# Performance work log

Hardware: AMD Instinct MI355X
Metric: run time of the kernel (lower is better)

The kernel has to match this reference:

```python
import jax, jax.numpy as jnp
import numpy as np

N_TYPES = 4
N_RELS = 8
N, E, IN_DIM, OUT_DIM = 100000, 1600000, 64, 64
SQRT_DK = float(np.sqrt(OUT_DIM))  # num_heads = 1 -> d_k = out_dim


def setup_inputs() -> dict:
    key = jax.random.key(0)
    ks = jax.random.split(key, 12)
    s = 0.05  # keep activations well-scaled (xavier-ish)
    h = jax.random.normal(ks[0], (N, IN_DIM), jnp.float32)
    node_type = jax.random.randint(ks[1], (N,), 0, N_TYPES, jnp.int32)
    src = jax.random.randint(ks[2], (E,), 0, N, jnp.int32)
    dst = jax.random.randint(ks[3], (E,), 0, N, jnp.int32)
    etype = jax.random.randint(ks[4], (E,), 0, N_RELS, jnp.int32)
    k_lin = jax.random.normal(ks[5], (N_TYPES, IN_DIM, OUT_DIM), jnp.float32) * s
    q_lin = jax.random.normal(ks[6], (N_TYPES, IN_DIM, OUT_DIM), jnp.float32) * s
    v_lin = jax.random.normal(ks[7], (N_TYPES, IN_DIM, OUT_DIM), jnp.float32) * s
    a_lin = jax.random.normal(ks[8], (N_TYPES, OUT_DIM, OUT_DIM), jnp.float32) * s
    rel_att = jax.random.normal(ks[9], (N_RELS, OUT_DIM, OUT_DIM), jnp.float32) * s
    rel_msg = jax.random.normal(ks[10], (N_RELS, OUT_DIM, OUT_DIM), jnp.float32) * s
    rel_pri = jnp.ones((N_RELS,), jnp.float32)
    skip = jnp.ones((N_TYPES,), jnp.float32)
    return dict(h=h, node_type=node_type, src=src, dst=dst, etype=etype,
                k_lin=k_lin, q_lin=q_lin, v_lin=v_lin, a_lin=a_lin,
                rel_att=rel_att, rel_msg=rel_msg, rel_pri=rel_pri, skip=skip)


def _typed_matmul(x, W, node_type):
    # rgnn_relational_matmul_no_scatter_gather_list: per-node-type GEMM.
    # Small fixed loop over node types (4), masked accumulate.
    out = jnp.zeros((x.shape[0], W.shape[-1]), x.dtype)
    for t in range(W.shape[0]):
        out = out + jnp.where((node_type == t)[:, None], x @ W[t], 0.0)
    return out


def reference(h, node_type, src, dst, etype, k_lin, q_lin, v_lin, a_lin,
              rel_att, rel_msg, rel_pri, skip):
    # per-node-type K/Q/V projections (num_heads==1, d_k==out_dim)
    k = _typed_matmul(h, k_lin, node_type)  # [N, d_k]
    q = _typed_matmul(h, q_lin, node_type)  # [N, d_k]
    v = _typed_matmul(h, v_lin, node_type)  # [N, d_k]

    # q @ relation_att, computed per relation for ALL nodes then gathered per edge
    # (avoids materializing [E, d_k, d_k] relation weights per edge)
    qW = jnp.einsum('nd,rde->rne', q, rel_att)  # [R, N, d_k]
    t_edge = qW[etype, dst]                      # [E, d_k]  (dst-side product)
    # attention score: <q_dst @ W_att_r, k_src>
    score = jnp.sum(t_edge * k[src], axis=-1)    # [E]

    # edge softmax over incoming edges of each dst, scaled by pri/sqrt(d_k)
    logits = score * (rel_pri / SQRT_DK)[etype]
    m = jax.ops.segment_max(logits, dst, num_segments=N)
    ex = jnp.exp(logits - m[dst])
    den = jax.ops.segment_sum(ex, dst, num_segments=N)
    alpha = ex / jnp.where(den[dst] == 0, 1.0, den[dst])  # [E]

    # message: v_src @ W_msg_r, per relation then gathered per edge
    vW = jnp.einsum('nd,rde->rne', v, rel_msg)   # [R, N, d_k]
    msg = vW[etype, src]                          # [E, d_k]

    # softmax-weighted aggregation to dst nodes
    agg = jax.ops.segment_sum(alpha[:, None] * msg, dst, num_segments=N)  # [N, d_k]

    # output per-node-type GEMM with sigmoid(skip)-scaled a_linears
    W_out = jax.nn.sigmoid(skip)[:, None, None] * a_lin
    return _typed_matmul(agg, W_out, node_type)  # [N, out_dim]
```

## Files before the change

kernel.cpp:

```cpp
#include <hip/hip_runtime.h>
#include <math.h>

#define DIM 64
#define NT 4
#define NR 8

typedef __attribute__((ext_vector_type(8))) short bf16x8;
typedef __attribute__((ext_vector_type(8))) unsigned short u16x8;
typedef __attribute__((ext_vector_type(4))) float f32x4;

__device__ __forceinline__ unsigned short f2bf(float f) {
    unsigned u = __float_as_uint(f);
    return (unsigned short)((u + 0x7FFF + ((u >> 16) & 1)) >> 16);
}
__device__ __forceinline__ float bf2f(unsigned short u) {
    return __uint_as_float((unsigned)u << 16);
}
__device__ __forceinline__ bf16x8 ldb16(const unsigned short* p) {
    return *((const bf16x8*)p);
}

__global__ void prep_all(const float* __restrict__ A, const float* __restrict__ Mw,
                         const float* __restrict__ kl, const float* __restrict__ ql,
                         const float* __restrict__ vl,
                         unsigned short* __restrict__ At, unsigned short* __restrict__ Mt,
                         unsigned short* __restrict__ Wkt, unsigned short* __restrict__ Wqt,
                         unsigned short* __restrict__ Wvt,
                         int* __restrict__ cnt8, int* __restrict__ tm, int M) {
    int i = blockIdx.x * blockDim.x + threadIdx.x;
    if (i < M) cnt8[i] = 0;
    if (i < 16) tm[i] = 0;
    if (i >= 28 * DIM * DIM) return;
    int mat = i >> 12;
    int idx = i & 4095;
    int n = idx >> 6;
    int k = idx & 63;
    int so = k * DIM + n;
    if (mat < 8)       At [((size_t)mat << 12) + idx]        = f2bf(A [((size_t)mat << 12) + so]);
    else if (mat < 16) Mt [((size_t)(mat - 8) << 12) + idx]  = f2bf(Mw[((size_t)(mat - 8) << 12) + so]);
    else if (mat < 20) Wkt[((size_t)(mat - 16) << 12) + idx] = f2bf(kl[((size_t)(mat - 16) << 12) + so]);
    else if (mat < 24) Wqt[((size_t)(mat - 20) << 12) + idx] = f2bf(ql[((size_t)(mat - 20) << 12) + so]);
    else               Wvt[((size_t)(mat - 24) << 12) + idx] = f2bf(vl[((size_t)(mat - 24) << 12) + so]);
}

__global__ void type_count(const int* __restrict__ ntype, int* __restrict__ tm,
                           int* __restrict__ order, int N, int ocap) {
    int i = blockIdx.x * blockDim.x + threadIdx.x;
    if (i < ocap) order[i] = -1;
    int t = (i < N) ? ntype[i] : -1;
    int lane = threadIdx.x & 63;
    #pragma unroll
    for (int tt = 0; tt < NT; tt++) {
        unsigned long long m = __ballot(t == tt);
        int c = __popcll(m);
        if (c && lane == (__ffsll((long long)m) - 1)) atomicAdd(&tm[tt], c);
    }
}

__global__ void type_scan(int* __restrict__ tm) {
    if (threadIdx.x == 0 && blockIdx.x == 0) {
        int b = 0;
        for (int t = 0; t < NT; t++) { tm[4 + t] = b; b += ((tm[t] + 63) >> 6) << 6; }
        tm[12] = b;
    }
}

__global__ void type_scatter(const int* __restrict__ ntype, int* __restrict__ tm,
                             int* __restrict__ order, int N) {
    int i = blockIdx.x * blockDim.x + threadIdx.x;
    int t = (i < N) ? ntype[i] : -1;
    int lane = threadIdx.x & 63;
    #pragma unroll
    for (int tt = 0; tt < NT; tt++) {
        unsigned long long m = __ballot(t == tt);
        int c = __popcll(m);
        if (!c) continue;
        int ldr = __ffsll((long long)m) - 1;
        int base = 0;
        if (lane == ldr) base = atomicAdd(&tm[8 + tt], c);
        base = __shfl(base, ldr, 64);
        if (t == tt) {
            int rank = __popcll(m & ((1ull << lane) - 1ull));
            order[tm[4 + tt] + base + rank] = i;
        }
    }
}

__global__ void __launch_bounds__(256)
proj_mfma(const float* __restrict__ h, const int* __restrict__ ntype,
          const int* __restrict__ order, const int* __restrict__ tm,
          const unsigned short* __restrict__ Wkt, const unsigned short* __restrict__ Wqt,
          const unsigned short* __restrict__ Wvt,
          unsigned short* __restrict__ kvbf, unsigned short* __restrict__ qbf, int N) {
    __shared__ __align__(16) unsigned short xs[64][72];
    int t  = threadIdx.x;
    int n0 = blockIdx.x * 64;
    if (n0 >= tm[12]) return;
    int first = order[n0];
    if (first < 0) return;
    int ty = ntype[first];

    int grow[2];
    #pragma unroll
    for (int i = 0; i < 2; i++) grow[i] = order[n0 + (t + 256 * i) / 8];

    #pragma unroll
    for (int i = 0; i < 4; i++) {
        int idx = t + 256 * i;
        int row = idx >> 4, c4 = idx & 15;
        int gn = order[n0 + row];
        float4 xv = make_float4(0.f, 0.f, 0.f, 0.f);
        if (gn >= 0) xv = ((const float4*)(h + (size_t)gn * DIM))[c4];
        ushort4 b = make_ushort4(f2bf(xv.x), f2bf(xv.y), f2bf(xv.z), f2bf(xv.w));
        *((ushort4*)&xs[row][c4 * 4]) = b;
    }
    __syncthreads();

    int wave = t >> 6, lane = t & 63;
    int m = lane & 15, quad = lane >> 4;
    bf16x8 xa0 = *((const bf16x8*)&xs[wave * 16 + m][quad * 8]);
    bf16x8 xa1 = *((const bf16x8*)&xs[wave * 16 + m][32 + quad * 8]);

    const unsigned short* Wt[3] = { Wkt + (size_t)ty * 4096,
                                    Wqt + (size_t)ty * 4096,
                                    Wvt + (size_t)ty * 4096 };
    for (int mm = 0; mm < 3; mm++) {
        const unsigned short* W = Wt[mm];
        f32x4 c0 = {0.f,0.f,0.f,0.f}, c1 = c0, c2 = c0, c3 = c0;
        c0 = __builtin_amdgcn_mfma_f32_16x16x32_bf16(xa0, ldb16(W + (( 0 + m) << 6)      + quad * 8), c0, 0, 0, 0);
        c1 = __builtin_amdgcn_mfma_f32_16x16x32_bf16(xa0, ldb16(W + ((16 + m) << 6)      + quad * 8), c1, 0, 0, 0);
        c2 = __builtin_amdgcn_mfma_f32_16x16x32_bf16(xa0, ldb16(W + ((32 + m) << 6)      + quad * 8), c2, 0, 0, 0);
        c3 = __builtin_amdgcn_mfma_f32_16x16x32_bf16(xa0, ldb16(W + ((48 + m) << 6)      + quad * 8), c3, 0, 0, 0);
        c0 = __builtin_amdgcn_mfma_f32_16x16x32_bf16(xa1, ldb16(W + (( 0 + m) << 6) + 32 + quad * 8), c0, 0, 0, 0);
        c1 = __builtin_amdgcn_mfma_f32_16x16x32_bf16(xa1, ldb16(W + ((16 + m) << 6) + 32 + quad * 8), c1, 0, 0, 0);
        c2 = __builtin_amdgcn_mfma_f32_16x16x32_bf16(xa1, ldb16(W + ((32 + m) << 6) + 32 + quad * 8), c2, 0, 0, 0);
        c3 = __builtin_amdgcn_mfma_f32_16x16x32_bf16(xa1, ldb16(W + ((48 + m) << 6) + 32 + quad * 8), c3, 0, 0, 0);

        __syncthreads();
        #pragma unroll
        for (int reg = 0; reg < 4; reg++) {
            unsigned short* qr = &xs[wave * 16 + quad * 4 + reg][m];
            qr[ 0] = f2bf(c0[reg]); qr[16] = f2bf(c1[reg]);
            qr[32] = f2bf(c2[reg]); qr[48] = f2bf(c3[reg]);
        }
        __syncthreads();
        #pragma unroll
        for (int i = 0; i < 2; i++) {
            int idx = t + 256 * i;
            int row = idx >> 3, c8 = idx & 7;
            int gn = grow[i];
            if (gn >= 0) {
                u16x8 v = *((const u16x8*)&xs[row][c8 * 8]);
                unsigned short* dp;
                if (mm == 1)      dp = qbf  + ((size_t)gn << 6) + c8 * 8;
                else if (mm == 0) dp = kvbf + ((size_t)gn << 7) + c8 * 8;
                else              dp = kvbf + ((size_t)gn << 7) + 64 + c8 * 8;
                *((u16x8*)dp) = v;
            }
        }
    }
}

__global__ void hist8(const int* __restrict__ dst, const int* __restrict__ et,
                      int* __restrict__ cnt, int* __restrict__ rank, int E) {
    int e = blockIdx.x * blockDim.x + threadIdx.x;
    if (e < E) rank[e] = atomicAdd(&cnt[dst[e] * NR + et[e]], 1);
}

__global__ void scan1(const int* __restrict__ cnt, int* __restrict__ off,
                      int* __restrict__ bsum, int M) {
    __shared__ int wsum[16];
    int tid = threadIdx.x;
    int lane = tid & 63, wid = tid >> 6;
    int i = blockIdx.x * 1024 + tid;
    int x0 = (i < M) ? cnt[i] : 0;
    int x = x0;
    #pragma unroll
    for (int s = 1; s < 64; s <<= 1) {
        int y = __shfl_up(x, s, 64);
        if (lane >= s) x += y;
    }
    if (lane == 63) wsum[wid] = x;
    __syncthreads();
    if (tid < 16) {
        int w = wsum[tid];
        #pragma unroll
        for (int s = 1; s < 16; s <<= 1) {
            int y = __shfl_up(w, s, 16);
            if (tid >= s) w += y;
        }
        wsum[tid] = w;
    }
    __syncthreads();
    int add = (wid > 0) ? wsum[wid - 1] : 0;
    if (i < M) off[i] = add + x - x0;
    if (tid == 1023) bsum[blockIdx.x] = wsum[15];
}

__global__ void scan2(int* __restrict__ bsum, int nb) {
    __shared__ int wsum[16];
    __shared__ int carry;
    int tid = threadIdx.x;
    int lane = tid & 63, wid = tid >> 6;
    if (tid == 0) carry = 0;
    __syncthreads();
    for (int base = 0; base < nb; base += 1024) {
        int i = base + tid;
        int x0 = (i < nb) ? bsum[i] : 0;
        int x = x0;
        #pragma unroll
        for (int s = 1; s < 64; s <<= 1) {
            int y = __shfl_up(x, s, 64);
            if (lane >= s) x += y;
        }
        if (lane == 63) wsum[wid] = x;
        __syncthreads();
        if (tid < 16) {
            int w = wsum[tid];
            #pragma unroll
            for (int s = 1; s < 16; s <<= 1) {
                int y = __shfl_up(w, s, 16);
                if (tid >= s) w += y;
            }
            wsum[tid] = w;
        }
        __syncthreads();
        int add = carry + ((wid > 0) ? wsum[wid - 1] : 0);
        if (i < nb) bsum[i] = add + x - x0;
        __syncthreads();
        if (tid == 0) carry += wsum[15];
        __syncthreads();
    }
}

__global__ void scan3(int* __restrict__ off, const int* __restrict__ bsum, int M, int E) {
    int i = blockIdx.x * 1024 + threadIdx.x;
    if (i < M) off[i] += bsum[blockIdx.x];
    if (i == 0) off[M] = E;
}

__global__ void scatter8(const int* __restrict__ src, const int* __restrict__ dst,
                         const int* __restrict__ et, const int* __restrict__ off,
                         const int* __restrict__ rank, int* __restrict__ se, int E) {
    int e = blockIdx.x * blockDim.x + threadIdx.x;
    if (e >= E) return;
    int key = dst[e] * NR + et[e];
    se[off[key] + rank[e]] = src[e];
}

__global__ void __launch_bounds__(256)
fused_edge(const unsigned short* __restrict__ qbf,
           const unsigned short* __restrict__ kvbf,
           const unsigned short* __restrict__ At,
           const unsigned short* __restrict__ Mt,
           const int* __restrict__ se, const int* __restrict__ off8,
           const float* __restrict__ rel_pri,
           float* __restrict__ agg, int N) {
    __shared__ __align__(16) unsigned short qwb[4][16][72];
    __shared__ __align__(16) unsigned short pl[4][16][72];
    const int t    = threadIdx.x;
    const int wave = t >> 6;
    const int lane = t & 63;
    const int m    = lane & 15;
    const int quad = lane >> 4;
    const int sg   = lane >> 2;
    const int ll   = lane & 3;
    const int n0   = blockIdx.x * 64 + wave * 16;
    if (n0 >= N) return;

    bf16x8 qa0 = {0,0,0,0,0,0,0,0}, qa1 = {0,0,0,0,0,0,0,0};
    {
        const int gn = n0 + m;
        if (gn < N) {
            const unsigned short* qp = qbf + ((size_t)gn << 6) + quad * 8;
            qa0 = *((const bf16x8*)qp);
            qa1 = *((const bf16x8*)(qp + 32));
        }
    }

    const int ob = n0 * NR;
    const int ov0 = off8[ob + lane];
    const int ov1 = off8[ob + 64 + lane];
    const int eeidx = ((n0 + 16 < N) ? (n0 + 16) : N) * NR;
    const int ov2 = off8[eeidx];
    const bool act = (n0 + sg) < N;

    f32x4 u0 = {0.f,0.f,0.f,0.f}, u1 = u0, u2 = u0, u3 = u0;
    float ddsum = 0.f;

    for (int r = 0; r < NR; r++) {
        const unsigned short* Ar = At + ((size_t)r << 12);
        f32x4 c0 = {0.f,0.f,0.f,0.f}, c1 = c0, c2 = c0, c3 = c0;
        c0 = __builtin_amdgcn_mfma_f32_16x16x32_bf16(qa0, ldb16(Ar + (( 0 + m) << 6)      + quad * 8), c0, 0, 0, 0);
        c1 = __builtin_amdgcn_mfma_f32_16x16x32_bf16(qa0, ldb16(Ar + ((16 + m) << 6)      + quad * 8), c1, 0, 0, 0);
        c2 = __builtin_amdgcn_mfma_f32_16x16x32_bf16(qa0, ldb16(Ar + ((32 + m) << 6)      + quad * 8), c2, 0, 0, 0);
        c3 = __builtin_amdgcn_mfma_f32_16x16x32_bf16(qa0, ldb16(Ar + ((48 + m) << 6)      + quad * 8), c3, 0, 0, 0);
        c0 = __builtin_amdgcn_mfma_f32_16x16x32_bf16(qa1, ldb16(Ar + (( 0 + m) << 6) + 32 + quad * 8), c0, 0, 0, 0);
        c1 = __builtin_amdgcn_mfma_f32_16x16x32_bf16(qa1, ldb16(Ar + ((16 + m) << 6) + 32 + quad * 8), c1, 0, 0, 0);
        c2 = __builtin_amdgcn_mfma_f32_16x16x32_bf16(qa1, ldb16(Ar + ((32 + m) << 6) + 32 + quad * 8), c2, 0, 0, 0);
        c3 = __builtin_amdgcn_mfma_f32_16x16x32_bf16(qa1, ldb16(Ar + ((48 + m) << 6) + 32 + quad * 8), c3, 0, 0, 0);

        #pragma unroll
        for (int reg = 0; reg < 4; reg++) {
            unsigned short* qr = &qwb[wave][quad * 4 + reg][m];
            qr[ 0] = f2bf(c0[reg]); qr[16] = f2bf(c1[reg]);
            qr[32] = f2bf(c2[reg]); qr[48] = f2bf(c3[reg]);
        }
        asm volatile("s_waitcnt lgkmcnt(0)" ::: "memory");

        const int g  = sg * NR + r;
        const int g1 = g + 1;
        const int x0a = __shfl(ov0, g, 64);
        const int x0b = __shfl(ov1, g - 64, 64);
        int i0 = (g < 64) ? x0a : x0b;
        const int x1a = __shfl(ov0, g1, 64);
        const int x1b = __shfl(ov1, g1 - 64, 64);
        int i1 = (g1 < 64) ? x1a : ((g1 < 128) ? x1b : ov2);
        if (!act) i1 = i0;

        const float pri = rel_pri[r] * 0.125f;
        float P[16];
        #pragma unroll
        for (int x = 0; x < 16; x++) P[x] = 0.f;
        float dd = 0.f;

        if (i0 < i1) {
            const u16x8 tq0 = *((const u16x8*)&qwb[wave][sg][ll * 16]);
            const u16x8 tq1 = *((const u16x8*)&qwb[wave][sg][ll * 16 + 8]);
            float tq[16];
            #pragma unroll
            for (int x = 0; x < 8; x++) { tq[x] = bf2f(tq0[x]); tq[8 + x] = bf2f(tq1[x]); }

            for (int i = i0; i < i1; i += 2) {
                const int sA = se[i];
                const bool hB = (i + 1 < i1);
                const int sB = se[hB ? i + 1 : i];
                const unsigned short* pA = kvbf + ((size_t)sA << 7) + ll * 16;
                const unsigned short* pB = kvbf + ((size_t)sB << 7) + ll * 16;
                const u16x8 kA0 = *((const u16x8*)pA);
                const u16x8 kA1 = *((const u16x8*)(pA + 8));
                const u16x8 vA0 = *((const u16x8*)(pA + 64));
                const u16x8 vA1 = *((const u16x8*)(pA + 72));
                const u16x8 kB0 = *((const u16x8*)pB);
                const u16x8 kB1 = *((const u16x8*)(pB + 8));
                const u16x8 vB0 = *((const u16x8*)(pB + 64));
                const u16x8 vB1 = *((const u16x8*)(pB + 72));
                float sa = 0.f, sb = 0.f;
                #pragma unroll
                for (int x = 0; x < 8; x++) {
                    sa = fmaf(bf2f(kA0[x]), tq[x],     sa);
                    sa = fmaf(bf2f(kA1[x]), tq[8 + x], sa);
                    sb = fmaf(bf2f(kB0[x]), tq[x],     sb);
                    sb = fmaf(bf2f(kB1[x]), tq[8 + x], sb);
                }
                sa += __shfl_xor(sa, 1, 4);
                sa += __shfl_xor(sa, 2, 4);
                sb += __shfl_xor(sb, 1, 4);
                sb += __shfl_xor(sb, 2, 4);
                const float eA = __expf(sa * pri);
                const float eB = hB ? __expf(sb * pri) : 0.f;
                dd += eA + eB;
                #pragma unroll
                for (int x = 0; x < 8; x++) {
                    P[x]     = fmaf(eA, bf2f(vA0[x]), P[x]);
                    P[8 + x] = fmaf(eA, bf2f(vA1[x]), P[8 + x]);
                    P[x]     = fmaf(eB, bf2f(vB0[x]), P[x]);
                    P[8 + x] = fmaf(eB, bf2f(vB1[x]), P[8 + x]);
                }
            }
        }
        u16x8 w0, w1;
        #pragma unroll
        for (int x = 0; x < 8; x++) {
            w0[x] = f2bf(P[x]);
            w1[x] = f2bf(P[8 + x]);
        }
        *((u16x8*)&pl[wave][sg][ll * 16])     = w0;
        *((u16x8*)&pl[wave][sg][ll * 16 + 8]) = w1;
        ddsum += dd;
        asm volatile("s_waitcnt lgkmcnt(0)" ::: "memory");

        const unsigned short* Mr = Mt + ((size_t)r << 12);
        const bf16x8 pa0 = *((const bf16x8*)&pl[wave][m][quad * 8]);
        const bf16x8 pa1 = *((const bf16x8*)&pl[wave][m][32 + quad * 8]);
        u0 = __builtin_amdgcn_mfma_f32_16x16x32_bf16(pa0, ldb16(Mr + (( 0 + m) << 6)      + quad * 8), u0, 0, 0, 0);
        u1 = __builtin_amdgcn_mfma_f32_16x16x32_bf16(pa0, ldb16(Mr + ((16 + m) << 6)      + quad * 8), u1, 0, 0, 0);
        u2 = __builtin_amdgcn_mfma_f32_16x16x32_bf16(pa0, ldb16(Mr + ((32 + m) << 6)      + quad * 8), u2, 0, 0, 0);
        u3 = __builtin_amdgcn_mfma_f32_16x16x32_bf16(pa0, ldb16(Mr + ((48 + m) << 6)      + quad * 8), u3, 0, 0, 0);
        u0 = __builtin_amdgcn_mfma_f32_16x16x32_bf16(pa1, ldb16(Mr + (( 0 + m) << 6) + 32 + quad * 8), u0, 0, 0, 0);
        u1 = __builtin_amdgcn_mfma_f32_16x16x32_bf16(pa1, ldb16(Mr + ((16 + m) << 6) + 32 + quad * 8), u1, 0, 0, 0);
        u2 = __builtin_amdgcn_mfma_f32_16x16x32_bf16(pa1, ldb16(Mr + ((32 + m) << 6) + 32 + quad * 8), u2, 0, 0, 0);
        u3 = __builtin_amdgcn_mfma_f32_16x16x32_bf16(pa1, ldb16(Mr + ((48 + m) << 6) + 32 + quad * 8), u3, 0, 0, 0);
        asm volatile("s_waitcnt lgkmcnt(0)" ::: "memory");
    }

    #pragma unroll
    for (int reg = 0; reg < 4; reg++) {
        const int n = n0 + quad * 4 + reg;
        if (n >= N) continue;
        const float dv  = __shfl(ddsum, (quad * 4 + reg) << 2, 64);
        const float inv = (dv == 0.f) ? 0.f : 1.f / dv;
        float* rowp = agg + ((size_t)n << 6) + m;
        rowp[ 0] = u0[reg] * inv;
        rowp[16] = u1[reg] * inv;
        rowp[32] = u2[reg] * inv;
        rowp[48] = u3[reg] * inv;
    }
}

__global__ void out_typed(const float* __restrict__ agg, const int* __restrict__ ntype,
                          const int* __restrict__ order, const int* __restrict__ tm,
                          const float* __restrict__ Wa, const float* __restrict__ skip,
                          float* __restrict__ out, int N) {
    __shared__ float xs[64][68];
    __shared__ float wsm[64][64];
    int t  = threadIdx.x;
    int n0 = blockIdx.x * 64;
    if (n0 >= tm[12]) return;
    int first = order[n0];
    if (first < 0) return;
    int ty = ntype[first];
    float sg = 1.f / (1.f + expf(-skip[ty]));

    const float4* wg = (const float4*)(Wa + (size_t)ty * DIM * DIM);
    float4* wl = (float4*)&wsm[0][0];
    #pragma unroll
    for (int i = 0; i < 4; i++) {
        float4 w = wg[t + 256 * i];
        w.x *= sg; w.y *= sg; w.z *= sg; w.w *= sg;
        wl[t + 256 * i] = w;
    }
    #pragma unroll
    for (int i = 0; i < 4; i++) {
        int idx = t + 256 * i;
        int row = idx >> 4, c4 = idx & 15;
        int gn = order[n0 + row];
        float4 xv = make_float4(0.f, 0.f, 0.f, 0.f);
        if (gn >= 0) xv = ((const float4*)(agg + (size_t)gn * DIM))[c4];
        ((float4*)&xs[row][0])[c4] = xv;
    }
    __syncthreads();

    int og  = t & 15;
    int ng4 = (t >> 4) * 4;
    float4 a0 = make_float4(0.f,0.f,0.f,0.f), a1 = a0, a2 = a0, a3 = a0;
    #pragma unroll 8
    for (int d = 0; d < DIM; d++) {
        float4 wv = ((const float4*)&wsm[d][0])[og];
        float x0 = xs[ng4 + 0][d];
        float x1 = xs[ng4 + 1][d];
        float x2 = xs[ng4 + 2][d];
        float x3 = xs[ng4 + 3][d];
        a0.x = fmaf(x0, wv.x, a0.x); a0.y = fmaf(x0, wv.y, a0.y);
        a0.z = fmaf(x0, wv.z, a0.z); a0.w = fmaf(x0, wv.w, a0.w);
        a1.x = fmaf(x1, wv.x, a1.x); a1.y = fmaf(x1, wv.y, a1.y);
        a1.z = fmaf(x1, wv.z, a1.z); a1.w = fmaf(x1, wv.w, a1.w);
        a2.x = fmaf(x2, wv.x, a2.x); a2.y = fmaf(x2, wv.y, a2.y);
        a2.z = fmaf(x2, wv.z, a2.z); a2.w = fmaf(x2, wv.w, a2.w);
        a3.x = fmaf(x3, wv.x, a3.x); a3.y = fmaf(x3, wv.y, a3.y);
        a3.z = fmaf(x3, wv.z, a3.z); a3.w = fmaf(x3, wv.w, a3.w);
    }
    int g0 = order[n0 + ng4 + 0];
    int g1 = order[n0 + ng4 + 1];
    int g2 = order[n0 + ng4 + 2];
    int g3 = order[n0 + ng4 + 3];
    if (g0 >= 0) ((float4*)(out + (size_t)g0 * DIM))[og] = a0;
    if (g1 >= 0) ((float4*)(out + (size_t)g1 * DIM))[og] = a1;
    if (g2 >= 0) ((float4*)(out + (size_t)g2 * DIM))[og] = a2;
    if (g3 >= 0) ((float4*)(out + (size_t)g3 * DIM))[og] = a3;
}

extern "C" void kernel_launch(void* const* d_in, const int* in_sizes, int n_in,
                              void* d_out, int out_size, void* d_ws, size_t ws_size,
                              hipStream_t stream) {
    const float* h       = (const float*)d_in[0];
    const int*   ntype   = (const int*)  d_in[1];
    const int*   src     = (const int*)  d_in[2];
    const int*   dst     = (const int*)  d_in[3];
    const int*   et      = (const int*)  d_in[4];
    const float* k_lin   = (const float*)d_in[5];
    const float* q_lin   = (const float*)d_in[6];
    const float* v_lin   = (const float*)d_in[7];
    const float* a_lin   = (const float*)d_in[8];
    const float* rel_att = (const float*)d_in[9];
    const float* rel_msg = (const float*)d_in[10];
    const float* rel_pri = (const float*)d_in[11];
    const float* skip    = (const float*)d_in[12];

    int N = in_sizes[1];
    int E = in_sizes[2];
    int M = N * NR;
    int ocap = N + NT * 64;

    float* ws = (float*)d_ws;
    size_t o = 0;
    unsigned short* kvbf = (unsigned short*)(ws + o); o += (size_t)N * DIM;
    unsigned short* qbf  = (unsigned short*)(ws + o); o += (size_t)N * DIM / 2;
    float* agg  = ws + o; o += (size_t)N * DIM;
    int* off8   = (int*)(ws + o); o += (size_t)M + 1024;
    int* cnt8   = (int*)(ws + o); o += (size_t)M;
    int* rank   = (int*)(ws + o); o += (size_t)E;
    int* se     = (int*)(ws + o); o += (size_t)E;
    int* bsum   = (int*)(ws + o); o += 1024;
    int* order  = (int*)(ws + o); o += (size_t)ocap;
    int* tm     = (int*)(ws + o); o += 16;
    unsigned short* At  = (unsigned short*)(ws + o); o += (size_t)NR * DIM * DIM / 2;
    unsigned short* Mt  = (unsigned short*)(ws + o); o += (size_t)NR * DIM * DIM / 2;
    unsigned short* Wkt = (unsigned short*)(ws + o); o += (size_t)NT * DIM * DIM / 2;
    unsigned short* Wqt = (unsigned short*)(ws + o); o += (size_t)NT * DIM * DIM / 2;
    unsigned short* Wvt = (unsigned short*)(ws + o); o += (size_t)NT * DIM * DIM / 2;

    float* out = (float*)d_out;

    int gprep = (M > 28 * DIM * DIM ? M : 28 * DIM * DIM);
    prep_all<<<(gprep + 255) / 256, 256, 0, stream>>>(
        rel_att, rel_msg, k_lin, q_lin, v_lin, At, Mt, Wkt, Wqt, Wvt, cnt8, tm, M);

    type_count<<<(ocap + 255) / 256, 256, 0, stream>>>(ntype, tm, order, N, ocap);
    type_scan<<<1, 64, 0, stream>>>(tm);
    type_scatter<<<(N + 255) / 256, 256, 0, stream>>>(ntype, tm, order, N);

    int gridT = (N + NT * 64 + 63) / 64;
    proj_mfma<<<gridT, 256, 0, stream>>>(h, ntype, order, tm, Wkt, Wqt, Wvt,
                                         kvbf, qbf, N);

    hist8<<<(E + 255) / 256, 256, 0, stream>>>(dst, et, cnt8, rank, E);
    int nb = (M + 1023) / 1024;
    scan1<<<nb, 1024, 0, stream>>>(cnt8, off8, bsum, M);
    scan2<<<1, 1024, 0, stream>>>(bsum, nb);
    scan3<<<nb, 1024, 0, stream>>>(off8, bsum, M, E);
    scatter8<<<(E + 255) / 256, 256, 0, stream>>>(src, dst, et, off8, rank, se, E);

    int nb64 = (N + 63) / 64;
    fused_edge<<<nb64, 256, 0, stream>>>(qbf, kvbf, At, Mt, se, off8,
                                         rel_pri, agg, N);

    out_typed<<<gridT, 256, 0, stream>>>(agg, ntype, order, tm, a_lin, skip, out, N);
}
```

Measured before the change: 595.1 us.

## Fuse output typed GEMM into edge kernel using type-sorted node order

The edge aggregation kernel now walks nodes in type-sorted order (q stored in sorted slots), so each 64-node block shares one node type. This lets the per-type output GEMM run in the same kernel from shared memory instead of writing agg to global memory and launching a separate out_typed kernel. It removes the agg round-trip and one launch. The cost is more shared memory per block (reduced occupancy) and gathered off8 and edge reads in sorted order, which lose some locality.

```diff
diff --git a/kernel.cpp b/kernel.cpp
--- a/kernel.cpp
+++ b/kernel.cpp
@@ -148,14 +148,17 @@
         for (int i = 0; i < 2; i++) {
             int idx = t + 256 * i;
             int row = idx >> 3, c8 = idx & 7;
-            int gn = grow[i];
-            if (gn >= 0) {
-                u16x8 v = *((const u16x8*)&xs[row][c8 * 8]);
-                unsigned short* dp;
-                if (mm == 1)      dp = qbf  + ((size_t)gn << 6) + c8 * 8;
-                else if (mm == 0) dp = kvbf + ((size_t)gn << 7) + c8 * 8;
-                else              dp = kvbf + ((size_t)gn << 7) + 64 + c8 * 8;
-                *((u16x8*)dp) = v;
+            u16x8 v = *((const u16x8*)&xs[row][c8 * 8]);
+            if (mm == 1) {
+                *((u16x8*)(qbf + ((size_t)(n0 + row) << 6) + c8 * 8)) = v;
+            } else {
+                int gn = grow[i];
+                if (gn >= 0) {
+                    unsigned short* dp = (mm == 0)
+                        ? kvbf + ((size_t)gn << 7) + c8 * 8
+                        : kvbf + ((size_t)gn << 7) + 64 + c8 * 8;
+                    *((u16x8*)dp) = v;
+                }
             }
         }
     }
@@ -255,9 +258,14 @@
            const unsigned short* __restrict__ Mt,
            const int* __restrict__ se, const int* __restrict__ off8,
            const float* __restrict__ rel_pri,
-           float* __restrict__ agg, int N) {
-    __shared__ __align__(16) unsigned short qwb[4][16][72];
-    __shared__ __align__(16) unsigned short pl[4][16][72];
+           const int* __restrict__ ntype, const int* __restrict__ order,
+           const int* __restrict__ tm,
+           const float* __restrict__ Wa, const float* __restrict__ skip,
+           float* __restrict__ out, int N) {
+    __shared__ __align__(16) unsigned short smem[2][4][16][72];
+    __shared__ __align__(16) float W2[64][64];
+    unsigned short (*qwb)[16][72] = smem[0];
+    unsigned short (*pl)[16][72]  = smem[1];
     const int t    = threadIdx.x;
     const int wave = t >> 6;
     const int lane = t & 63;
@@ -266,24 +274,34 @@
     const int sg   = lane >> 2;
     const int ll   = lane & 3;
     const int n0   = blockIdx.x * 64 + wave * 16;
-    if (n0 >= N) return;
-
-    bf16x8 qa0 = {0,0,0,0,0,0,0,0}, qa1 = {0,0,0,0,0,0,0,0};
-    {
-        const int gn = n0 + m;
-        if (gn < N) {
-            const unsigned short* qp = qbf + ((size_t)gn << 6) + quad * 8;
-            qa0 = *((const bf16x8*)qp);
-            qa1 = *((const bf16x8*)(qp + 32));
-        }
-    }
-
-    const int ob = n0 * NR;
-    const int ov0 = off8[ob + lane];
-    const int ov1 = off8[ob + 64 + lane];
-    const int eeidx = ((n0 + 16 < N) ? (n0 + 16) : N) * NR;
-    const int ov2 = off8[eeidx];
-    const bool act = (n0 + sg) < N;
+    const int tot  = tm[12];
+    const bool blkvalid = (blockIdx.x * 64) < tot;
+
+    if (blkvalid) {
+        const int ty = ntype[order[blockIdx.x * 64]];
+        const float sgs = 1.f / (1.f + expf(-skip[ty]));
+        const float4* wg = (const float4*)(Wa + (size_t)ty * DIM * DIM);
+        float4* wl = (float4*)&W2[0][0];
+        #pragma unroll
+        for (int i = 0; i < 4; i++) {
+            float4 w = wg[t + 256 * i];
+            w.x *= sgs; w.y *= sgs; w.z *= sgs; w.w *= sgs;
+            wl[t + 256 * i] = w;
+        }
+    }
+    __syncthreads();
+    if (!blkvalid) return;
+
+    const int nid = order[n0 + sg];
+    const bool act = nid >= 0;
+    const int nb8 = act ? nid * NR : 0;
+    const int ovA = off8[nb8 + ll * 2];
+    const int ovB = off8[nb8 + ll * 2 + 1];
+    const int ovC = off8[nb8 + 8];
+
+    const unsigned short* qp = qbf + ((size_t)(n0 + m) << 6) + quad * 8;
+    const bf16x8 qa0 = *((const bf16x8*)qp);
+    const bf16x8 qa1 = *((const bf16x8*)(qp + 32));
 
     f32x4 u0 = {0.f,0.f,0.f,0.f}, u1 = u0, u2 = u0, u3 = u0;
     float ddsum = 0.f;
@@ -308,14 +326,15 @@
         }
         asm volatile("s_waitcnt lgkmcnt(0)" ::: "memory");
 
-        const int g  = sg * NR + r;
-        const int g1 = g + 1;
-        const int x0a = __shfl(ov0, g, 64);
-        const int x0b = __shfl(ov1, g - 64, 64);
-        int i0 = (g < 64) ? x0a : x0b;
-        const int x1a = __shfl(ov0, g1, 64);
-        const int x1b = __shfl(ov1, g1 - 64, 64);
-        int i1 = (g1 < 64) ? x1a : ((g1 < 128) ? x1b : ov2);
+        const int bl0 = (sg << 2) | (r >> 1);
+        const int va  = __shfl(ovA, bl0, 64);
+        const int vb  = __shfl(ovB, bl0, 64);
+        const int i0  = (r & 1) ? vb : va;
+        const int rr  = r + 1;
+        const int bl1 = ((sg << 2) | ((rr >> 1) & 3));
+        const int wa2 = __shfl(ovA, bl1, 64);
+        const int wb2 = __shfl(ovB, bl1, 64);
+        int i1 = (rr == 8) ? ovC : ((rr & 1) ? wb2 : wa2);
         if (!act) i1 = i0;
 
         const float pri = rel_pri[r] * 0.125f;
@@ -394,63 +413,32 @@
         asm volatile("s_waitcnt lgkmcnt(0)" ::: "memory");
     }
 
+    __syncthreads();
+    float* Ut = (float*)&smem[0][0][0][0];
     #pragma unroll
     for (int reg = 0; reg < 4; reg++) {
-        const int n = n0 + quad * 4 + reg;
-        if (n >= N) continue;
-        const float dv  = __shfl(ddsum, (quad * 4 + reg) << 2, 64);
+        const int row = quad * 4 + reg;
+        const float dv  = __shfl(ddsum, row << 2, 64);
         const float inv = (dv == 0.f) ? 0.f : 1.f / dv;
-        float* rowp = agg + ((size_t)n << 6) + m;
-        rowp[ 0] = u0[reg] * inv;
-        rowp[16] = u1[reg] * inv;
-        rowp[32] = u2[reg] * inv;
-        rowp[48] = u3[reg] * inv;
-    }
-}
-
-__global__ void out_typed(const float* __restrict__ agg, const int* __restrict__ ntype,
-                          const int* __restrict__ order, const int* __restrict__ tm,
-                          const float* __restrict__ Wa, const float* __restrict__ skip,
-                          float* __restrict__ out, int N) {
-    __shared__ float xs[64][68];
-    __shared__ float wsm[64][64];
-    int t  = threadIdx.x;
-    int n0 = blockIdx.x * 64;
-    if (n0 >= tm[12]) return;
-    int first = order[n0];
-    if (first < 0) return;
-    int ty = ntype[first];
-    float sg = 1.f / (1.f + expf(-skip[ty]));
-
-    const float4* wg = (const float4*)(Wa + (size_t)ty * DIM * DIM);
-    float4* wl = (float4*)&wsm[0][0];
-    #pragma unroll
-    for (int i = 0; i < 4; i++) {
-        float4 w = wg[t + 256 * i];
-        w.x *= sg; w.y *= sg; w.z *= sg; w.w *= sg;
-        wl[t + 256 * i] = w;
-    }
-    #pragma unroll
-    for (int i = 0; i < 4; i++) {
-        int idx = t + 256 * i;
-        int row = idx >> 4, c4 = idx & 15;
-        int gn = order[n0 + row];
-        float4 xv = make_float4(0.f, 0.f, 0.f, 0.f);
-        if (gn >= 0) xv = ((const float4*)(agg + (size_t)gn * DIM))[c4];
-        ((float4*)&xs[row][0])[c4] = xv;
-    }
-    __syncthreads();
-
-    int og  = t & 15;
-    int ng4 = (t >> 4) * 4;
+        float* rp = Ut + ((size_t)(wave * 16 + row)) * 68 + m;
+        rp[ 0] = u0[reg] * inv;
+        rp[16] = u1[reg] * inv;
+        rp[32] = u2[reg] * inv;
+        rp[48] = u3[reg] * inv;
+    }
+    asm volatile("s_waitcnt lgkmcnt(0)" ::: "memory");
+
+    const int og  = lane & 15;
+    const int ng4 = (lane >> 4) * 4;
     float4 a0 = make_float4(0.f,0.f,0.f,0.f), a1 = a0, a2 = a0, a3 = a0;
+    const float* xb = Ut + ((size_t)(wave * 16 + ng4)) * 68;
     #pragma unroll 8
     for (int d = 0; d < DIM; d++) {
-        float4 wv = ((const float4*)&wsm[d][0])[og];
-        float x0 = xs[ng4 + 0][d];
-        float x1 = xs[ng4 + 1][d];
-        float x2 = xs[ng4 + 2][d];
-        float x3 = xs[ng4 + 3][d];
+        float4 wv = *((const float4*)&W2[d][og * 4]);
+        float x0 = xb[d];
+        float x1 = xb[68 + d];
+        float x2 = xb[136 + d];
+        float x3 = xb[204 + d];
         a0.x = fmaf(x0, wv.x, a0.x); a0.y = fmaf(x0, wv.y, a0.y);
         a0.z = fmaf(x0, wv.z, a0.z); a0.w = fmaf(x0, wv.w, a0.w);
         a1.x = fmaf(x1, wv.x, a1.x); a1.y = fmaf(x1, wv.y, a1.y);
@@ -460,10 +448,10 @@
         a3.x = fmaf(x3, wv.x, a3.x); a3.y = fmaf(x3, wv.y, a3.y);
         a3.z = fmaf(x3, wv.z, a3.z); a3.w = fmaf(x3, wv.w, a3.w);
     }
-    int g0 = order[n0 + ng4 + 0];
-    int g1 = order[n0 + ng4 + 1];
-    int g2 = order[n0 + ng4 + 2];
-    int g3 = order[n0 + ng4 + 3];
+    const int g0 = order[n0 + ng4 + 0];
+    const int g1 = order[n0 + ng4 + 1];
+    const int g2 = order[n0 + ng4 + 2];
+    const int g3 = order[n0 + ng4 + 3];
     if (g0 >= 0) ((float4*)(out + (size_t)g0 * DIM))[og] = a0;
     if (g1 >= 0) ((float4*)(out + (size_t)g1 * DIM))[og] = a1;
     if (g2 >= 0) ((float4*)(out + (size_t)g2 * DIM))[og] = a2;
@@ -495,8 +483,7 @@
     float* ws = (float*)d_ws;
     size_t o = 0;
     unsigned short* kvbf = (unsigned short*)(ws + o); o += (size_t)N * DIM;
-    unsigned short* qbf  = (unsigned short*)(ws + o); o += (size_t)N * DIM / 2;
-    float* agg  = ws + o; o += (size_t)N * DIM;
+    unsigned short* qbf  = (unsigned short*)(ws + o); o += (size_t)ocap * DIM / 2;
     int* off8   = (int*)(ws + o); o += (size_t)M + 1024;
     int* cnt8   = (int*)(ws + o); o += (size_t)M;
     int* rank   = (int*)(ws + o); o += (size_t)E;
@@ -531,9 +518,6 @@
     scan3<<<nb, 1024, 0, stream>>>(off8, bsum, M, E);
     scatter8<<<(E + 255) / 256, 256, 0, stream>>>(src, dst, et, off8, rank, se, E);
 
-    int nb64 = (N + 63) / 64;
-    fused_edge<<<nb64, 256, 0, stream>>>(qbf, kvbf, At, Mt, se, off8,
-                                         rel_pri, agg, N);
-
-    out_typed<<<gridT, 256, 0, stream>>>(agg, ntype, order, tm, a_lin, skip, out, N);
-}
+    fused_edge<<<gridT, 256, 0, stream>>>(qbf, kvbf, At, Mt, se, off8, rel_pri,
+                                          ntype, order, tm, a_lin, skip, out, N);
+}
```

After: 590.5 us, median of 2. About the same (-0.8%).
